# Performance work log

Hardware: AMD Instinct MI355X
Metric: run time of the kernel (lower is better)

The kernel has to match this reference:

```python
import jax, jax.numpy as jnp
import numpy as np

N_NODES = 100000


def gcn_conv(x, W, b, src, dst, n_nodes):
    # GCNConv: h = x @ W; add self-loops; symmetric norm; aggregate; + bias
    h = x @ W  # [N, out]
    loop = jnp.arange(n_nodes, dtype=src.dtype)
    s = jnp.concatenate([src, loop])  # source of each message
    d = jnp.concatenate([dst, loop])  # target of each message
    ones = jnp.ones(d.shape[0], dtype=x.dtype)
    deg = jax.ops.segment_sum(ones, d, num_segments=n_nodes)  # in-degree incl. self-loop
    dinv = jnp.where(deg > 0, jax.lax.rsqrt(deg), 0.0)
    norm = dinv[s] * dinv[d]  # [E+N]
    msg = h[s] * norm[:, None]  # gather + scale
    out = jax.ops.segment_sum(msg, d, num_segments=n_nodes)  # scatter-add
    return out + b


def setup_inputs() -> dict:
    key = jax.random.key(0)
    k1, k2, k3, k4, k5 = jax.random.split(key, 5)
    nfeat, nhid, nclass = 128, 128, 40
    x = jax.random.normal(k1, (N_NODES, nfeat), dtype=jnp.float32)
    edge_index = jax.random.randint(k2, (2, 640000), 0, N_NODES, dtype=jnp.int64)
    # Glorot-style init for conv weights, zero bias (PyG defaults)
    W1 = jax.random.normal(k3, (nfeat, nhid), dtype=jnp.float32) * (1.0 / np.sqrt(nfeat))
    b1 = jnp.zeros((nhid,), dtype=jnp.float32)
    W2 = jax.random.normal(k4, (nhid, nclass), dtype=jnp.float32) * (1.0 / np.sqrt(nhid))
    b2 = jnp.zeros((nclass,), dtype=jnp.float32)
    return {"x": x, "edge_index": edge_index, "W1": W1, "b1": b1, "W2": W2, "b2": b2}


def reference(x, edge_index, W1, b1, W2, b2):
    src, dst = edge_index[0], edge_index[1]
    n = x.shape[0]
    # layer 1 + relu (dropout is identity at inference)
    h = gcn_conv(x, W1, b1, src, dst, n)
    h = jax.nn.relu(h)
    # final layer (no activation)
    out = gcn_conv(h, W2, b2, src, dst, n)
    return out
```

## Files before the change

kernel.cpp:

```cpp
#include <hip/hip_runtime.h>
#include <stdint.h>

#define N_NODES 100000
#define NB 782
#define NBP 784
#define BCAP 1536
#define EPB 12800

typedef __attribute__((ext_vector_type(8))) short bf16x8;
typedef __attribute__((ext_vector_type(4))) float f32x4;
typedef __attribute__((ext_vector_type(4))) unsigned short u16x4;
typedef __attribute__((ext_vector_type(8))) unsigned short u16x8;

__device__ __forceinline__ unsigned short f2bf(float f){
    uint32_t u = __float_as_uint(f);
    uint32_t r = (u + 0x7FFFu + ((u >> 16) & 1u)) >> 16;
    return (unsigned short)r;
}
__device__ __forceinline__ float bf2f(unsigned short h){
    return __uint_as_float(((uint32_t)h) << 16);
}

__global__ void to_bf16_v8(const float* __restrict__ in, unsigned short* __restrict__ outp, int n8){
    int i = blockIdx.x * 256 + threadIdx.x;
    if (i < n8){
        float4 a = ((const float4*)in)[2 * i];
        float4 b = ((const float4*)in)[2 * i + 1];
        u16x8 o = { f2bf(a.x), f2bf(a.y), f2bf(a.z), f2bf(a.w),
                    f2bf(b.x), f2bf(b.y), f2bf(b.z), f2bf(b.w) };
        ((u16x8*)outp)[i] = o;
    }
}

__global__ void transpose_w_frag2(const float* __restrict__ W1, unsigned short* __restrict__ Wtf1,
                                  const float* __restrict__ W2, unsigned short* __restrict__ Wtf2){
    const int T1 = 8 * 4 * 64 * 8;
    const int T2 = 3 * 4 * 64 * 8;
    int i = blockIdx.x * 256 + threadIdx.x;
    if (i < T1){
        int j = i & 7, l = (i >> 3) & 63, st = (i >> 9) & 3, cb = i >> 11;
        int k = st * 32 + (l >> 4) * 8 + j, col = cb * 16 + (l & 15);
        Wtf1[i] = f2bf(W1[(size_t)k * 128 + col]);
    } else if (i < T1 + T2){
        int i2 = i - T1;
        int j = i2 & 7, l = (i2 >> 3) & 63, st = (i2 >> 9) & 3, cb = i2 >> 11;
        int k = st * 32 + (l >> 4) * 8 + j, col = cb * 16 + (l & 15);
        Wtf2[i2] = f2bf((col < 40) ? W2[(size_t)k * 40 + col] : 0.f);
    }
}

__global__ __launch_bounds__(1024) void bucket_hist_priv(const int* __restrict__ dst,
        uint32_t* __restrict__ ghist, int E){
    __shared__ uint32_t h[NBP];
    for (int i = threadIdx.x; i < NBP; i += 1024) h[i] = 0u;
    __syncthreads();
    int base = blockIdx.x * EPB;
    for (int i = threadIdx.x; i < EPB; i += 1024){
        int e = base + i;
        if (e < E) atomicAdd(&h[(uint32_t)dst[e] >> 7], 1u);
    }
    __syncthreads();
    for (int i = threadIdx.x; i < NBP; i += 1024)
        ghist[blockIdx.x * NBP + i] = h[i];
}

__global__ __launch_bounds__(1024) void scan_buckets2(const uint32_t* __restrict__ ghist,
        uint32_t* __restrict__ base, uint32_t* __restrict__ hist,
        uint32_t* __restrict__ stg, int nblk){
    __shared__ uint32_t tmp[1024];
    int t = threadIdx.x;
    uint32_t tot = 0u;
    if (t < NB){
        for (int b = 0; b < nblk; b++) tot += ghist[b * NBP + t];
        hist[t] = tot;
    }
    tmp[t] = (t < NB) ? tot : 0u;
    __syncthreads();
    for (int off = 1; off < 1024; off <<= 1){
        uint32_t v = (t >= off) ? tmp[t - off] : 0u;
        __syncthreads();
        tmp[t] += v;
        __syncthreads();
    }
    if (t < NB){
        uint32_t ex = tmp[t] - tot;
        base[t] = ex;
        uint32_t run = ex;
        for (int b = 0; b < nblk; b++){
            stg[b * NBP + t] = run;
            run += ghist[b * NBP + t];
        }
    }
}

__global__ __launch_bounds__(1024) void bucket_scatter2(const int* __restrict__ src,
        const int* __restrict__ dst, const uint32_t* __restrict__ stg,
        uint32_t* __restrict__ ebuf, int E){
    __shared__ uint32_t rank[NBP];
    __shared__ uint32_t stl[NBP];
    int bl = blockIdx.x;
    for (int i = threadIdx.x; i < NBP; i += 1024){
        rank[i] = 0u;
        stl[i] = stg[bl * NBP + i];
    }
    __syncthreads();
    int base = bl * EPB;
    for (int i = threadIdx.x; i < EPB; i += 1024){
        int e = base + i;
        if (e < E){
            uint32_t d = (uint32_t)dst[e];
            uint32_t b = d >> 7;
            uint32_t r = atomicAdd(&rank[b], 1u);
            ebuf[stl[b] + r] = ((d & 127u) << 17) | (uint32_t)src[e];
        }
    }
}

__global__ __launch_bounds__(256) void bucket_csr(const uint32_t* __restrict__ hist,
        const uint32_t* __restrict__ base, const uint32_t* __restrict__ ebuf,
        uint32_t* __restrict__ offs, uint32_t* __restrict__ cnt, float* __restrict__ dinv,
        uint32_t* __restrict__ slot, int N){
    __shared__ uint32_t ebl[BCAP];
    __shared__ uint32_t ncnt[128], loff[128], ncur[128], stmp[128];
    int b = blockIdx.x, t = threadIdx.x;
    uint32_t eb = base[b], ec = hist[b];
    if (ec > BCAP) ec = BCAP;
    for (uint32_t i = t; i < ec; i += 256) ebl[i] = ebuf[eb + i];
    if (t < 128){ ncnt[t] = 0u; ncur[t] = 0u; }
    __syncthreads();
    for (uint32_t i = t; i < ec; i += 256) atomicAdd(&ncnt[ebl[i] >> 17], 1u);
    __syncthreads();
    if (t < 128) stmp[t] = ncnt[t];
    __syncthreads();
    for (int off = 1; off < 128; off <<= 1){
        uint32_t v = 0u;
        if (t < 128 && t >= off) v = stmp[t - off];
        __syncthreads();
        if (t < 128) stmp[t] += v;
        __syncthreads();
    }
    if (t < 128) loff[t] = stmp[t] - ncnt[t];
    __syncthreads();
    int g = b * 128 + t;
    if (t < 128 && g < N){
        offs[g] = eb + loff[t];
        cnt[g]  = ncnt[t];
        dinv[g] = rsqrtf((float)(ncnt[t] + 1u));
    }
    for (uint32_t i = t; i < ec; i += 256){
        uint32_t p  = ebl[i];
        uint32_t ld = p >> 17;
        uint32_t r  = atomicAdd(&ncur[ld], 1u);
        slot[eb + loff[ld] + r] = p & 0x1FFFFu;
    }
}

__global__ __launch_bounds__(256) void agg_bf(const unsigned short* __restrict__ Xh,
        const uint32_t* __restrict__ offs, const uint32_t* __restrict__ cnt,
        const uint32_t* __restrict__ slot, const float* __restrict__ dinv,
        unsigned short* __restrict__ OUT){
    int wgid = blockIdx.x * 4 + (threadIdx.x >> 6);
    int lane = threadIdx.x & 63;
    int h = lane >> 5, l = lane & 31;
    int g = wgid * 2 + h;
    const u16x4* X4 = (const u16x4*)Xh;
    uint32_t o = offs[g], c = cnt[g];
    float ax = 0.f, ay = 0.f, az = 0.f, aw = 0.f;
    #pragma unroll 1
    for (uint32_t base = 0; base < c; base += 32){
        int rem = (int)(c - base); if (rem > 32) rem = 32;
        uint32_t idx = 0u; float ds = 0.f;
        if (l < rem){
            idx = slot[o + base + (uint32_t)l];
            ds = dinv[idx];
        }
        int groups = (rem + 7) >> 3;
        #pragma unroll 1
        for (int gq = 0; gq < groups; gq++){
            int eb = gq * 8;
            u16x4 v[8]; float d[8];
            #pragma unroll
            for (int j = 0; j < 8; j++){
                uint32_t s = (uint32_t)__shfl((int)idx, eb + j, 32);
                d[j] = __shfl(ds, eb + j, 32);
                v[j] = X4[(size_t)s * 32 + l];
            }
            #pragma unroll
            for (int j = 0; j < 8; j++){
                ax += d[j] * bf2f(v[j][0]);
                ay += d[j] * bf2f(v[j][1]);
                az += d[j] * bf2f(v[j][2]);
                aw += d[j] * bf2f(v[j][3]);
            }
        }
    }
    float dd = dinv[g];
    u16x4 sv = X4[(size_t)g * 32 + l];
    u16x4 r = { f2bf(dd * (ax + dd * bf2f(sv[0]))),
                f2bf(dd * (ay + dd * bf2f(sv[1]))),
                f2bf(dd * (az + dd * bf2f(sv[2]))),
                f2bf(dd * (aw + dd * bf2f(sv[3]))) };
    ((u16x4*)OUT)[(size_t)g * 32 + l] = r;
}

__global__ __launch_bounds__(256) void gemm_mfma_l1(const unsigned short* __restrict__ Xagg,
        const unsigned short* __restrict__ Wtf, const float* __restrict__ bias,
        unsigned short* __restrict__ OUT){
    int tid = threadIdx.x;
    int wid = tid >> 6, l = tid & 63;
    int lm = l & 15, lk = l >> 4;
    int rw = blockIdx.x * 64 + wid * 16;
    int ra = rw + lm; ra = ra < N_NODES ? ra : N_NODES - 1;
    const bf16x8* Wv = (const bf16x8*)Wtf;

    f32x4 acc[8] = {};
    bf16x8 aA, aB, bA[8], bB[8];

    aA = *(const bf16x8*)(Xagg + (size_t)ra * 128 + lk * 8);
    #pragma unroll
    for (int cb = 0; cb < 8; cb++) bA[cb] = Wv[(size_t)(cb * 4 + 0) * 64 + l];

    aB = *(const bf16x8*)(Xagg + (size_t)ra * 128 + 32 + lk * 8);
    #pragma unroll
    for (int cb = 0; cb < 8; cb++) bB[cb] = Wv[(size_t)(cb * 4 + 1) * 64 + l];
    #pragma unroll
    for (int cb = 0; cb < 8; cb++)
        acc[cb] = __builtin_amdgcn_mfma_f32_16x16x32_bf16(aA, bA[cb], acc[cb], 0, 0, 0);

    aA = *(const bf16x8*)(Xagg + (size_t)ra * 128 + 64 + lk * 8);
    #pragma unroll
    for (int cb = 0; cb < 8; cb++) bA[cb] = Wv[(size_t)(cb * 4 + 2) * 64 + l];
    #pragma unroll
    for (int cb = 0; cb < 8; cb++)
        acc[cb] = __builtin_amdgcn_mfma_f32_16x16x32_bf16(aB, bB[cb], acc[cb], 0, 0, 0);

    aB = *(const bf16x8*)(Xagg + (size_t)ra * 128 + 96 + lk * 8);
    #pragma unroll
    for (int cb = 0; cb < 8; cb++) bB[cb] = Wv[(size_t)(cb * 4 + 3) * 64 + l];
    #pragma unroll
    for (int cb = 0; cb < 8; cb++)
        acc[cb] = __builtin_amdgcn_mfma_f32_16x16x32_bf16(aA, bA[cb], acc[cb], 0, 0, 0);

    #pragma unroll
    for (int cb = 0; cb < 8; cb++)
        acc[cb] = __builtin_amdgcn_mfma_f32_16x16x32_bf16(aB, bB[cb], acc[cb], 0, 0, 0);

    #pragma unroll
    for (int cb = 0; cb < 8; cb++){
        int col = cb * 16 + lm;
        float bs = bias[col];
        #pragma unroll
        for (int i = 0; i < 4; i++){
            int row = rw + lk * 4 + i;
            if (row < N_NODES)
                OUT[(size_t)row * 128 + col] = f2bf(fmaxf(acc[cb][i] + bs, 0.f));
        }
    }
}

__global__ __launch_bounds__(256) void gemm_mfma_l2(const unsigned short* __restrict__ Aagg,
        const unsigned short* __restrict__ Wtf, const float* __restrict__ bias,
        float* __restrict__ OUT){
    int tid = threadIdx.x;
    int wid = tid >> 6, l = tid & 63;
    int lm = l & 15, lk = l >> 4;
    int rw = blockIdx.x * 64 + wid * 16;
    int ra = rw + lm; ra = ra < N_NODES ? ra : N_NODES - 1;
    const bf16x8* Wv = (const bf16x8*)Wtf;

    f32x4 acc[3] = {};
    bf16x8 aA, aB, bA[3], bB[3];

    aA = *(const bf16x8*)(Aagg + (size_t)ra * 128 + lk * 8);
    #pragma unroll
    for (int cb = 0; cb < 3; cb++) bA[cb] = Wv[(size_t)(cb * 4 + 0) * 64 + l];

    aB = *(const bf16x8*)(Aagg + (size_t)ra * 128 + 32 + lk * 8);
    #pragma unroll
    for (int cb = 0; cb < 3; cb++) bB[cb] = Wv[(size_t)(cb * 4 + 1) * 64 + l];
    #pragma unroll
    for (int cb = 0; cb < 3; cb++)
        acc[cb] = __builtin_amdgcn_mfma_f32_16x16x32_bf16(aA, bA[cb], acc[cb], 0, 0, 0);

    aA = *(const bf16x8*)(Aagg + (size_t)ra * 128 + 64 + lk * 8);
    #pragma unroll
    for (int cb = 0; cb < 3; cb++) bA[cb] = Wv[(size_t)(cb * 4 + 2) * 64 + l];
    #pragma unroll
    for (int cb = 0; cb < 3; cb++)
        acc[cb] = __builtin_amdgcn_mfma_f32_16x16x32_bf16(aB, bB[cb], acc[cb], 0, 0, 0);

    aB = *(const bf16x8*)(Aagg + (size_t)ra * 128 + 96 + lk * 8);
    #pragma unroll
    for (int cb = 0; cb < 3; cb++) bB[cb] = Wv[(size_t)(cb * 4 + 3) * 64 + l];
    #pragma unroll
    for (int cb = 0; cb < 3; cb++)
        acc[cb] = __builtin_amdgcn_mfma_f32_16x16x32_bf16(aA, bA[cb], acc[cb], 0, 0, 0);

    #pragma unroll
    for (int cb = 0; cb < 3; cb++)
        acc[cb] = __builtin_amdgcn_mfma_f32_16x16x32_bf16(aB, bB[cb], acc[cb], 0, 0, 0);

    #pragma unroll
    for (int cb = 0; cb < 3; cb++){
        int col = cb * 16 + lm;
        if (col < 40){
            float bs = bias[col];
            #pragma unroll
            for (int i = 0; i < 4; i++){
                int row = rw + lk * 4 + i;
                if (row < N_NODES) OUT[(size_t)row * 40 + col] = acc[cb][i] + bs;
            }
        }
    }
}

extern "C" void kernel_launch(void* const* d_in, const int* in_sizes, int n_in,
                              void* d_out, int out_size, void* d_ws, size_t ws_size,
                              hipStream_t stream) {
    const float* x   = (const float*)d_in[0];
    const int*   ei  = (const int*)d_in[1];
    const float* W1  = (const float*)d_in[2];
    const float* b1  = (const float*)d_in[3];
    const float* W2  = (const float*)d_in[4];
    const float* b2  = (const float*)d_in[5];
    float*       out = (float*)d_out;

    const int N = N_NODES;
    const int E = in_sizes[1] / 2;
    const int* src = ei;
    const int* dst = ei + E;

    char* ws = (char*)d_ws;
    size_t o = 0;
    auto alloc = [&](size_t bytes) -> char* {
        char* p = ws + o;
        o += (bytes + 511) & ~(size_t)511;
        return p;
    };
    const int nblk_edge = (E + EPB - 1) / EPB;
    uint32_t*       ghist = (uint32_t*)alloc((size_t)nblk_edge * NBP * 4);
    uint32_t*       stg   = (uint32_t*)alloc((size_t)nblk_edge * NBP * 4);
    uint32_t*       hist  = (uint32_t*)alloc((size_t)NBP * 4);
    uint32_t*       bbase = (uint32_t*)alloc((size_t)NBP * 4);
    uint32_t*       ebuf  = (uint32_t*)alloc((size_t)E * 4);
    uint32_t*       offs  = (uint32_t*)alloc((size_t)N * 4);
    uint32_t*       cnt   = (uint32_t*)alloc((size_t)N * 4);
    uint32_t*       slot  = (uint32_t*)alloc((size_t)E * 4);
    float*          dinv  = (float*)alloc((size_t)N * 4);
    unsigned short* Wtf1  = (unsigned short*)alloc((size_t)8 * 4 * 64 * 8 * 2);
    unsigned short* Wtf2  = (unsigned short*)alloc((size_t)3 * 4 * 64 * 8 * 2);
    unsigned short* Xh    = (unsigned short*)alloc((size_t)N * 128 * 2);
    unsigned short* Xagg  = (unsigned short*)alloc((size_t)N * 128 * 2);
    unsigned short* Ah    = (unsigned short*)alloc((size_t)N * 128 * 2);
    unsigned short* Aagg2 = Xh;

    const int n8 = N * 128 / 8;
    const int nblk_agg = N / 8;
    const int nblk_gemm = (N + 63) / 64;

    to_bf16_v8<<<(n8 + 255) / 256, 256, 0, stream>>>(x, Xh, n8);
    transpose_w_frag2<<<88, 256, 0, stream>>>(W1, Wtf1, W2, Wtf2);
    bucket_hist_priv<<<nblk_edge, 1024, 0, stream>>>(dst, ghist, E);
    scan_buckets2<<<1, 1024, 0, stream>>>(ghist, bbase, hist, stg, nblk_edge);
    bucket_scatter2<<<nblk_edge, 1024, 0, stream>>>(src, dst, stg, ebuf, E);
    bucket_csr<<<NB, 256, 0, stream>>>(hist, bbase, ebuf, offs, cnt, dinv, slot, N);

    agg_bf<<<nblk_agg, 256, 0, stream>>>(Xh, offs, cnt, slot, dinv, Xagg);
    gemm_mfma_l1<<<nblk_gemm, 256, 0, stream>>>(Xagg, Wtf1, b1, Ah);

    agg_bf<<<nblk_agg, 256, 0, stream>>>(Ah, offs, cnt, slot, dinv, Aagg2);
    gemm_mfma_l2<<<nblk_gemm, 256, 0, stream>>>(Aagg2, Wtf2, b2, out);
}
```

Measured before the change: 159.1 us.

## Fuse preamble kernels, shrink edge blocks, widen aggregation to 16-byte row loads

Three preamble kernels (x to bf16 conversion, weight fragment transpose, edge bucket histogram) are merged into one launch, with block ranges picking the role. Edges per block drop to 3200 and the histogram and scatter blocks go from 1024 to 256 threads, giving more, smaller blocks. Aggregation now uses 16 lanes per node with 8-bf16 (16-byte) loads, so each wavefront handles 4 nodes instead of 2. This targets launch overhead and gather efficiency, but scan_buckets2 now loops serially over four times as many per-block histograms.

```diff
diff --git a/kernel.cpp b/kernel.cpp
--- a/kernel.cpp
+++ b/kernel.cpp
@@ -5,11 +5,13 @@
 #define NB 782
 #define NBP 784
 #define BCAP 1536
-#define EPB 12800
+#define EPB 3200
+#define NBLK_CONV 6250
+#define NBLK_W 88
+#define NBLK_HIST 200
 
 typedef __attribute__((ext_vector_type(8))) short bf16x8;
 typedef __attribute__((ext_vector_type(4))) float f32x4;
-typedef __attribute__((ext_vector_type(4))) unsigned short u16x4;
 typedef __attribute__((ext_vector_type(8))) unsigned short u16x8;
 
 __device__ __forceinline__ unsigned short f2bf(float f){
@@ -21,47 +23,47 @@
     return __uint_as_float(((uint32_t)h) << 16);
 }
 
-__global__ void to_bf16_v8(const float* __restrict__ in, unsigned short* __restrict__ outp, int n8){
-    int i = blockIdx.x * 256 + threadIdx.x;
-    if (i < n8){
-        float4 a = ((const float4*)in)[2 * i];
-        float4 b = ((const float4*)in)[2 * i + 1];
+__global__ __launch_bounds__(256) void preamble(const float* __restrict__ x,
+        unsigned short* __restrict__ Xh,
+        const float* __restrict__ W1, unsigned short* __restrict__ Wtf1,
+        const float* __restrict__ W2, unsigned short* __restrict__ Wtf2,
+        const int* __restrict__ dst, uint32_t* __restrict__ ghist, int E){
+    __shared__ uint32_t h[NBP];
+    int bx = blockIdx.x, t = threadIdx.x;
+    if (bx < NBLK_CONV){
+        int i = bx * 256 + t;
+        float4 a = ((const float4*)x)[2 * i];
+        float4 b = ((const float4*)x)[2 * i + 1];
         u16x8 o = { f2bf(a.x), f2bf(a.y), f2bf(a.z), f2bf(a.w),
                     f2bf(b.x), f2bf(b.y), f2bf(b.z), f2bf(b.w) };
-        ((u16x8*)outp)[i] = o;
-    }
-}
-
-__global__ void transpose_w_frag2(const float* __restrict__ W1, unsigned short* __restrict__ Wtf1,
-                                  const float* __restrict__ W2, unsigned short* __restrict__ Wtf2){
-    const int T1 = 8 * 4 * 64 * 8;
-    const int T2 = 3 * 4 * 64 * 8;
-    int i = blockIdx.x * 256 + threadIdx.x;
-    if (i < T1){
-        int j = i & 7, l = (i >> 3) & 63, st = (i >> 9) & 3, cb = i >> 11;
-        int k = st * 32 + (l >> 4) * 8 + j, col = cb * 16 + (l & 15);
-        Wtf1[i] = f2bf(W1[(size_t)k * 128 + col]);
-    } else if (i < T1 + T2){
-        int i2 = i - T1;
-        int j = i2 & 7, l = (i2 >> 3) & 63, st = (i2 >> 9) & 3, cb = i2 >> 11;
-        int k = st * 32 + (l >> 4) * 8 + j, col = cb * 16 + (l & 15);
-        Wtf2[i2] = f2bf((col < 40) ? W2[(size_t)k * 40 + col] : 0.f);
-    }
-}
-
-__global__ __launch_bounds__(1024) void bucket_hist_priv(const int* __restrict__ dst,
-        uint32_t* __restrict__ ghist, int E){
-    __shared__ uint32_t h[NBP];
-    for (int i = threadIdx.x; i < NBP; i += 1024) h[i] = 0u;
-    __syncthreads();
-    int base = blockIdx.x * EPB;
-    for (int i = threadIdx.x; i < EPB; i += 1024){
-        int e = base + i;
-        if (e < E) atomicAdd(&h[(uint32_t)dst[e] >> 7], 1u);
-    }
-    __syncthreads();
-    for (int i = threadIdx.x; i < NBP; i += 1024)
-        ghist[blockIdx.x * NBP + i] = h[i];
+        ((u16x8*)Xh)[i] = o;
+    } else if (bx < NBLK_CONV + NBLK_W){
+        const int T1 = 8 * 4 * 64 * 8;
+        const int T2 = 3 * 4 * 64 * 8;
+        int i = (bx - NBLK_CONV) * 256 + t;
+        if (i < T1){
+            int j = i & 7, l = (i >> 3) & 63, st = (i >> 9) & 3, cb = i >> 11;
+            int k = st * 32 + (l >> 4) * 8 + j, col = cb * 16 + (l & 15);
+            Wtf1[i] = f2bf(W1[(size_t)k * 128 + col]);
+        } else if (i < T1 + T2){
+            int i2 = i - T1;
+            int j = i2 & 7, l = (i2 >> 3) & 63, st = (i2 >> 9) & 3, cb = i2 >> 11;
+            int k = st * 32 + (l >> 4) * 8 + j, col = cb * 16 + (l & 15);
+            Wtf2[i2] = f2bf((col < 40) ? W2[(size_t)k * 40 + col] : 0.f);
+        }
+    } else {
+        int bl = bx - NBLK_CONV - NBLK_W;
+        for (int i = t; i < NBP; i += 256) h[i] = 0u;
+        __syncthreads();
+        int base = bl * EPB;
+        for (int i = t; i < EPB; i += 256){
+            int e = base + i;
+            if (e < E) atomicAdd(&h[(uint32_t)dst[e] >> 7], 1u);
+        }
+        __syncthreads();
+        for (int i = t; i < NBP; i += 256)
+            ghist[bl * NBP + i] = h[i];
+    }
 }
 
 __global__ __launch_bounds__(1024) void scan_buckets2(const uint32_t* __restrict__ ghist,
@@ -93,19 +95,19 @@
     }
 }
 
-__global__ __launch_bounds__(1024) void bucket_scatter2(const int* __restrict__ src,
+__global__ __launch_bounds__(256) void bucket_scatter2(const int* __restrict__ src,
         const int* __restrict__ dst, const uint32_t* __restrict__ stg,
         uint32_t* __restrict__ ebuf, int E){
     __shared__ uint32_t rank[NBP];
     __shared__ uint32_t stl[NBP];
     int bl = blockIdx.x;
-    for (int i = threadIdx.x; i < NBP; i += 1024){
+    for (int i = threadIdx.x; i < NBP; i += 256){
         rank[i] = 0u;
         stl[i] = stg[bl * NBP + i];
     }
     __syncthreads();
     int base = bl * EPB;
-    for (int i = threadIdx.x; i < EPB; i += 1024){
+    for (int i = threadIdx.x; i < EPB; i += 256){
         int e = base + i;
         if (e < E){
             uint32_t d = (uint32_t)dst[e];
@@ -155,52 +157,52 @@
     }
 }
 
-__global__ __launch_bounds__(256) void agg_bf(const unsigned short* __restrict__ Xh,
+__global__ __launch_bounds__(256) void agg_bf4(const unsigned short* __restrict__ Xh,
         const uint32_t* __restrict__ offs, const uint32_t* __restrict__ cnt,
         const uint32_t* __restrict__ slot, const float* __restrict__ dinv,
         unsigned short* __restrict__ OUT){
     int wgid = blockIdx.x * 4 + (threadIdx.x >> 6);
-    int lane = threadIdx.x & 63;
-    int h = lane >> 5, l = lane & 31;
-    int g = wgid * 2 + h;
-    const u16x4* X4 = (const u16x4*)Xh;
+    int l = threadIdx.x & 63;
+    int ql = l & 15;
+    int g = wgid * 4 + (l >> 4);
+    const u16x8* X8 = (const u16x8*)Xh;
     uint32_t o = offs[g], c = cnt[g];
-    float ax = 0.f, ay = 0.f, az = 0.f, aw = 0.f;
+    float acc[8] = {};
     #pragma unroll 1
-    for (uint32_t base = 0; base < c; base += 32){
-        int rem = (int)(c - base); if (rem > 32) rem = 32;
+    for (uint32_t base = 0; base < c; base += 16){
+        int rem = (int)(c - base); if (rem > 16) rem = 16;
         uint32_t idx = 0u; float ds = 0.f;
-        if (l < rem){
-            idx = slot[o + base + (uint32_t)l];
+        if (ql < rem){
+            idx = slot[o + base + (uint32_t)ql];
             ds = dinv[idx];
         }
         int groups = (rem + 7) >> 3;
         #pragma unroll 1
         for (int gq = 0; gq < groups; gq++){
             int eb = gq * 8;
-            u16x4 v[8]; float d[8];
+            u16x8 v[8]; float d[8];
             #pragma unroll
             for (int j = 0; j < 8; j++){
-                uint32_t s = (uint32_t)__shfl((int)idx, eb + j, 32);
-                d[j] = __shfl(ds, eb + j, 32);
-                v[j] = X4[(size_t)s * 32 + l];
+                int srcl = (l & 48) | (eb + j);
+                uint32_t s = (uint32_t)__shfl((int)idx, srcl, 64);
+                d[j] = __shfl(ds, srcl, 64);
+                v[j] = X8[(size_t)s * 16 + ql];
             }
             #pragma unroll
             for (int j = 0; j < 8; j++){
-                ax += d[j] * bf2f(v[j][0]);
-                ay += d[j] * bf2f(v[j][1]);
-                az += d[j] * bf2f(v[j][2]);
-                aw += d[j] * bf2f(v[j][3]);
+                #pragma unroll
+                for (int f = 0; f < 8; f++)
+                    acc[f] += d[j] * bf2f(v[j][f]);
             }
         }
     }
     float dd = dinv[g];
-    u16x4 sv = X4[(size_t)g * 32 + l];
-    u16x4 r = { f2bf(dd * (ax + dd * bf2f(sv[0]))),
-                f2bf(dd * (ay + dd * bf2f(sv[1]))),
-                f2bf(dd * (az + dd * bf2f(sv[2]))),
-                f2bf(dd * (aw + dd * bf2f(sv[3]))) };
-    ((u16x4*)OUT)[(size_t)g * 32 + l] = r;
+    u16x8 sv = X8[(size_t)g * 16 + ql];
+    u16x8 r;
+    #pragma unroll
+    for (int f = 0; f < 8; f++)
+        r[f] = f2bf(dd * (acc[f] + dd * bf2f(sv[f])));
+    ((u16x8*)OUT)[(size_t)g * 16 + ql] = r;
 }
 
 __global__ __launch_bounds__(256) void gemm_mfma_l1(const unsigned short* __restrict__ Xagg,
@@ -354,20 +356,18 @@
     unsigned short* Ah    = (unsigned short*)alloc((size_t)N * 128 * 2);
     unsigned short* Aagg2 = Xh;
 
-    const int n8 = N * 128 / 8;
-    const int nblk_agg = N / 8;
+    const int nblk_agg = N / 16;
     const int nblk_gemm = (N + 63) / 64;
 
-    to_bf16_v8<<<(n8 + 255) / 256, 256, 0, stream>>>(x, Xh, n8);
-    transpose_w_frag2<<<88, 256, 0, stream>>>(W1, Wtf1, W2, Wtf2);
-    bucket_hist_priv<<<nblk_edge, 1024, 0, stream>>>(dst, ghist, E);
+    preamble<<<NBLK_CONV + NBLK_W + NBLK_HIST, 256, 0, stream>>>(
+        x, Xh, W1, Wtf1, W2, Wtf2, dst, ghist, E);
     scan_buckets2<<<1, 1024, 0, stream>>>(ghist, bbase, hist, stg, nblk_edge);
-    bucket_scatter2<<<nblk_edge, 1024, 0, stream>>>(src, dst, stg, ebuf, E);
+    bucket_scatter2<<<nblk_edge, 256, 0, stream>>>(src, dst, stg, ebuf, E);
     bucket_csr<<<NB, 256, 0, stream>>>(hist, bbase, ebuf, offs, cnt, dinv, slot, N);
 
-    agg_bf<<<nblk_agg, 256, 0, stream>>>(Xh, offs, cnt, slot, dinv, Xagg);
+    agg_bf4<<<nblk_agg, 256, 0, stream>>>(Xh, offs, cnt, slot, dinv, Xagg);
     gemm_mfma_l1<<<nblk_gemm, 256, 0, stream>>>(Xagg, Wtf1, b1, Ah);
 
-    agg_bf<<<nblk_agg, 256, 0, stream>>>(Ah, offs, cnt, slot, dinv, Aagg2);
+    agg_bf4<<<nblk_agg, 256, 0, stream>>>(Ah, offs, cnt, slot, dinv, Aagg2);
     gemm_mfma_l2<<<nblk_gemm, 256, 0, stream>>>(Aagg2, Wtf2, b2, out);
 }
```

After: 189.6 us. 1.19x slower.
